# Optimization experiments

Measured on AMD Instinct MI355X. Metric: run time of the kernel, lower is better.

Reference implementation:

```python
import jax, jax.numpy as jnp
import numpy as np

B, T, D = 64, 512, 256   # batch, time, input feat
H = 256                  # LSTM hidden (features)


def setup_inputs() -> dict:
    key = jax.random.key(0)
    ks = jax.random.split(key, 16)
    s = lambda k, shp, fan: jax.random.normal(k, shp, jnp.float32) / np.sqrt(fan)
    return {
        "x":  jax.random.normal(ks[0], (B, T, D), jnp.float32),
        # LSTM params: fused gates order (i, f, g, o)
        "Wi": s(ks[1], (D, 4 * H), D),
        "Wh": s(ks[2], (H, 4 * H), H),
        "b":  jnp.zeros((4 * H,), jnp.float32),
        # single-head attention (head_dim = H)
        "Wq": s(ks[3], (H, H), H), "bq": jnp.zeros((H,), jnp.float32),
        "Wk": s(ks[4], (H, H), H), "bk": jnp.zeros((H,), jnp.float32),
        "Wv": s(ks[5], (H, H), H), "bv": jnp.zeros((H,), jnp.float32),
        "Wo": s(ks[6], (H, H), H), "bo": jnp.zeros((H,), jnp.float32),
        # MLP head
        "W1": s(ks[7], (H, 32), H), "b1": jnp.zeros((32,), jnp.float32),
        "W2": s(ks[8], (32, 3), 32), "b2": jnp.zeros((3,), jnp.float32),
    }


def _lstm_scan(x, Wi, Wh, b):
    # Precompute input-to-hidden projection for all timesteps (batched GEMM)
    xg = jnp.einsum('btd,dg->btg', x, Wi) + b          # [B,T,4H]
    c0 = jnp.zeros((x.shape[0], Wh.shape[0]), x.dtype)
    h0 = jnp.zeros_like(c0)

    def step(carry, xg_t):
        c, h = carry
        g = xg_t + h @ Wh                               # [B,4H]
        i, f, gg, o = jnp.split(g, 4, axis=-1)          # flax gate order i,f,g,o
        c = jax.nn.sigmoid(f) * c + jax.nn.sigmoid(i) * jnp.tanh(gg)
        h = jax.nn.sigmoid(o) * jnp.tanh(c)
        return (c, h), h

    (_, _), hs = jax.lax.scan(step, (c0, h0), jnp.swapaxes(xg, 0, 1))
    return jnp.swapaxes(hs, 0, 1)                       # [B,T,H]


def reference(x, Wi, Wh, b, Wq, bq, Wk, bk, Wv, bv, Wo, bo, W1, b1, W2, b2):
    h = _lstm_scan(x, Wi, Wh, b)                        # [B,T,H]
    # single-head dot-product attention (self-attention)
    q = h @ Wq + bq
    k = h @ Wk + bk
    v = h @ Wv + bv
    scale = 1.0 / np.sqrt(q.shape[-1]).astype(np.float32)
    scores = jnp.einsum('bqd,bkd->bqk', q * scale, k)   # [B,T,T]
    attn = jax.nn.softmax(scores, axis=-1)
    o = jnp.einsum('bqk,bkd->bqd', attn, v)
    o = o @ Wo + bo                                     # output projection
    # head on first timestep
    z = jax.nn.relu(o[:, 0, :] @ W1 + b1)
    return z @ W2 + b2                                  # [B,3]
```

## Files before the change

### kernel.cpp

```cpp
#include <hip/hip_runtime.h>
#include <hip/hip_bf16.h>


typedef __attribute__((ext_vector_type(8))) short short8;
typedef __attribute__((ext_vector_type(4))) float float4v;

__device__ __forceinline__ unsigned short f2bf(float f) {
  unsigned u = __builtin_bit_cast(unsigned, f);
  return (unsigned short)((u + 0x7fffu + ((u >> 16) & 1u)) >> 16);
}
__device__ __forceinline__ float bf2f(unsigned short h) {
  return __builtin_bit_cast(float, ((unsigned)h) << 16);
}
__device__ __forceinline__ float bcl(unsigned u) {
  return __builtin_bit_cast(float, u << 16);
}
__device__ __forceinline__ float bch(unsigned u) {
  return __builtin_bit_cast(float, u & 0xffff0000u);
}
__device__ __forceinline__ float sigm(float x) { return 1.f / (1.f + __expf(-x)); }
__device__ __forceinline__ float tanh_f(float x) { return 1.f - 2.f / (1.f + __expf(2.f * x)); }

__global__ void prep_x(const float* __restrict__ x, unsigned short* __restrict__ xbf) {
  size_t i = ((size_t)blockIdx.x * 256 + threadIdx.x) * 4;
  float4 v = *(const float4*)&x[i];
  unsigned long long pk = (unsigned long long)f2bf(v.x)
                        | ((unsigned long long)f2bf(v.y) << 16)
                        | ((unsigned long long)f2bf(v.z) << 32)
                        | ((unsigned long long)f2bf(v.w) << 48);
  *(unsigned long long*)&xbf[i] = pk;
}

__global__ void prep_wit(const float* __restrict__ Wi, unsigned short* __restrict__ WiT) {
  size_t i = ((size_t)blockIdx.x * 256 + threadIdx.x) * 4;
  float4 v = *(const float4*)&Wi[i];
  int k = (int)(i >> 10), n = (int)(i & 1023);
  WiT[(size_t)(n + 0) * 256 + k] = f2bf(v.x);
  WiT[(size_t)(n + 1) * 256 + k] = f2bf(v.y);
  WiT[(size_t)(n + 2) * 256 + k] = f2bf(v.z);
  WiT[(size_t)(n + 3) * 256 + k] = f2bf(v.w);
}

__global__ void init_hx(unsigned long long* __restrict__ hx) {
  hx[(size_t)blockIdx.x * 256 + threadIdx.x] = 0xffffffff00000000ULL;
}

#define XKP 40
__global__ __launch_bounds__(256) void xg_gemm(const unsigned short* __restrict__ xbf,
                                               const unsigned short* __restrict__ WiT,
                                               const float* __restrict__ bias,
                                               unsigned short* __restrict__ xg) {
  __shared__ unsigned short As[128 * XKP];
  __shared__ unsigned short Bs[128 * XKP];
  const int tid = threadIdx.x;
  const int n0 = blockIdx.x * 128, m0 = blockIdx.y * 128;
  const int wave = tid >> 6, lane = tid & 63, quad = lane >> 4, l16 = lane & 15;
  const int wm = wave >> 1, wn = wave & 1;

  float4v acc[4][4];
#pragma unroll
  for (int i = 0; i < 4; ++i)
#pragma unroll
    for (int j = 0; j < 4; ++j) acc[i][j] = (float4v){0.f, 0.f, 0.f, 0.f};

  const int rr = tid >> 2, c8 = (tid & 3) * 8;
  for (int k0 = 0; k0 < 256; k0 += 32) {
#pragma unroll
    for (int pp = 0; pp < 2; ++pp) {
      int r = pp * 64 + rr;
      *(uint4*)&As[r * XKP + c8] = *(const uint4*)&xbf[(size_t)(m0 + r) * 256 + k0 + c8];
      *(uint4*)&Bs[r * XKP + c8] = *(const uint4*)&WiT[(size_t)(n0 + r) * 256 + k0 + c8];
    }
    __syncthreads();
#pragma unroll
    for (int mt = 0; mt < 4; ++mt) {
      short8 af = *(const short8*)&As[(wm * 64 + mt * 16 + l16) * XKP + quad * 8];
#pragma unroll
      for (int nt = 0; nt < 4; ++nt) {
        short8 bf = *(const short8*)&Bs[(wn * 64 + nt * 16 + l16) * XKP + quad * 8];
        acc[mt][nt] = __builtin_amdgcn_mfma_f32_16x16x32_bf16(af, bf, acc[mt][nt], 0, 0, 0);
      }
    }
    __syncthreads();
  }
#pragma unroll
  for (int nt = 0; nt < 4; ++nt) {
    int col = n0 + wn * 64 + nt * 16 + l16;
    int gate = col >> 8, ggx = (col >> 4) & 15, ul = col & 15;
    float bv = bias[col];
#pragma unroll
    for (int mt = 0; mt < 4; ++mt) {
#pragma unroll
      for (int r = 0; r < 4; ++r) {
        int row = m0 + wm * 64 + mt * 16 + quad * 4 + r;
        int b = row >> 9, t = row & 511;
        xg[(((size_t)ggx * 64 + b) * 512 + t) * 64 + gate * 16 + ul] =
            f2bf(acc[mt][nt][r] + bv);
      }
    }
  }
}

#define KP2 264
__global__ __launch_bounds__(256) void lstm_scan(const float* __restrict__ Wh,
                                                 const unsigned short* __restrict__ xgbuf,
                                                 unsigned short* __restrict__ hout,
                                                 unsigned long long* __restrict__ hx) {
  __shared__ unsigned short WhS[64 * KP2];
  __shared__ unsigned short hA[16 * KP2];
  __shared__ float preS[16 * 68];
  __shared__ float cS[256];
  const int tid = threadIdx.x;
  const int wg = blockIdx.x, bg = wg >> 4, gg = wg & 15;
  const int wave = tid >> 6, lane = tid & 63, quad = lane >> 4, l16 = lane & 15;

  {
    int uu = tid & 15, kh = tid >> 4;
#pragma unroll
    for (int gt = 0; gt < 4; ++gt)
      for (int kb = 0; kb < 16; ++kb) {
        int k = kb * 16 + kh;
        WhS[(gt * 16 + uu) * KP2 + k] = f2bf(Wh[(size_t)k * 1024 + gt * 256 + gg * 16 + uu]);
      }
  }
  for (int i = tid; i < 16 * KP2; i += 256) hA[i] = 0;
  cS[tid] = 0.f;
  __syncthreads();

  const int b_loc = tid >> 4, u_loc = tid & 15;
  const int bgb = bg * 16 + b_loc;
  const int u_glob = gg * 16 + u_loc;
  const int nrow = wave * 16 + l16;
  const unsigned short* xgp0 = xgbuf + ((size_t)(gg * 64 + bgb) * 512) * 64 + u_loc;

  unsigned short xi = xgp0[0], xf = xgp0[16], xG = xgp0[32], xo = xgp0[48];

  for (int t = 0; t < 512; ++t) {
    float4v acc = (float4v){0.f, 0.f, 0.f, 0.f};
#pragma unroll
    for (int kt = 0; kt < 8; ++kt) {
      short8 af = *(const short8*)&hA[l16 * KP2 + kt * 32 + quad * 8];
      short8 bf = *(const short8*)&WhS[nrow * KP2 + kt * 32 + quad * 8];
      acc = __builtin_amdgcn_mfma_f32_16x16x32_bf16(af, bf, acc, 0, 0, 0);
    }
#pragma unroll
    for (int r = 0; r < 4; ++r)
      preS[(quad * 4 + r) * 68 + wave * 16 + l16] = acc[r];

    int tn = (t < 511) ? t + 1 : t;
    const unsigned short* xgn = xgp0 + (size_t)tn * 64;
    unsigned short nxi = xgn[0], nxf = xgn[16], nxG = xgn[32], nxo = xgn[48];
    __syncthreads();

    float gi = preS[b_loc * 68 + 0 * 16 + u_loc] + bf2f(xi);
    float gf = preS[b_loc * 68 + 1 * 16 + u_loc] + bf2f(xf);
    float gG = preS[b_loc * 68 + 2 * 16 + u_loc] + bf2f(xG);
    float go = preS[b_loc * 68 + 3 * 16 + u_loc] + bf2f(xo);
    float c = sigm(gf) * cS[tid] + sigm(gi) * tanh_f(gG);
    cS[tid] = c;
    float h = sigm(go) * tanh_f(c);
    unsigned hb = (unsigned)f2bf(h);
    hA[b_loc * KP2 + u_glob] = (unsigned short)hb;

    const unsigned tg = (unsigned)t;
    unsigned v1 = __shfl_down((int)hb, 1);
    if ((u_loc & 1) == 0) {
      unsigned d0 = hb | (v1 << 16);
      unsigned long long val = (unsigned long long)d0 | ((unsigned long long)tg << 32);
      unsigned long long* dst =
          hx + (((size_t)(t & 1) * 64 + bgb) * 128 + (u_glob >> 1));
      __hip_atomic_store(dst, val, __ATOMIC_RELAXED, __HIP_MEMORY_SCOPE_AGENT);
      *(unsigned*)&hout[((size_t)bgb * 512 + t) * 256 + u_glob] = d0;
    }

    {
      int b2 = tid >> 4, grp = tid & 15;
      if (grp != gg) {
        const unsigned long long* base =
            hx + (((size_t)(t & 1) * 64 + bg * 16 + b2) * 128 + grp * 8);
        unsigned long long w[8];
        int guard = 0;
        bool ok;
        do {
          ok = true;
#pragma unroll
          for (int i = 0; i < 8; ++i) {
            w[i] = __hip_atomic_load(&base[i], __ATOMIC_RELAXED,
                                     __HIP_MEMORY_SCOPE_AGENT);
            ok &= ((unsigned)(w[i] >> 32) == tg);
          }
        } while (!ok && ++guard < (1 << 20));
        int u0 = grp * 16;
#pragma unroll
        for (int i = 0; i < 8; ++i)
          *(unsigned*)&hA[b2 * KP2 + u0 + 2 * i] = (unsigned)w[i];
      }
    }
    xi = nxi; xf = nxf; xG = nxG; xo = nxo;
    __syncthreads();
  }
}

__global__ __launch_bounds__(256) void attn_qu(const unsigned short* __restrict__ hout,
                                               const float* __restrict__ Wq,
                                               const float* __restrict__ bq,
                                               const float* __restrict__ Wk,
                                               const float* __restrict__ bk,
                                               float* __restrict__ us,
                                               float* __restrict__ cbuf) {
  __shared__ float h0S[256], q0S[256], red[256];
  const int b = blockIdx.x, tid = threadIdx.x;
  h0S[tid] = bf2f(hout[(size_t)b * 512 * 256 + tid]);
  __syncthreads();
  float a = 0.f;
  for (int k = 0; k < 256; ++k) a += h0S[k] * Wq[(size_t)k * 256 + tid];
  q0S[tid] = a + bq[tid];
  __syncthreads();
  red[tid] = q0S[tid] * bk[tid];
  __syncthreads();
  for (int s = 128; s > 0; s >>= 1) {
    if (tid < s) red[tid] += red[tid + s];
    __syncthreads();
  }
  if (tid == 0) cbuf[b] = 0.0625f * red[0];
  float acc = 0.f;
  const float* wr = &Wk[(size_t)tid * 256];
  for (int e = 0; e < 256; e += 4) {
    float4 w = *(const float4*)&wr[e];
    acc += w.x * q0S[e] + w.y * q0S[e + 1] + w.z * q0S[e + 2] + w.w * q0S[e + 3];
  }
  us[b * 256 + tid] = 0.0625f * acc;
}

__global__ __launch_bounds__(256) void attn_sm(const unsigned short* __restrict__ hout,
                                               const float* __restrict__ us,
                                               const float* __restrict__ cbuf,
                                               float* __restrict__ hbar) {
  __shared__ float sS[512], red[256], hb4[4][256];
  const int b = blockIdx.x, tid = threadIdx.x, wave = tid >> 6, lane = tid & 63;
  const size_t hb_base = (size_t)b * 512 * 256;
  const float u0 = us[b * 256 + lane * 4 + 0], u1 = us[b * 256 + lane * 4 + 1];
  const float u2 = us[b * 256 + lane * 4 + 2], u3 = us[b * 256 + lane * 4 + 3];
  const float cbv = cbuf[b];
  for (int i = 0; i < 128; ++i) {
    int t = i * 4 + wave;
    unsigned long long hv = *(const unsigned long long*)&hout[hb_base + (size_t)t * 256 + lane * 4];
    unsigned lo = (unsigned)hv, hi = (unsigned)(hv >> 32);
    float p = u0 * bcl(lo) + u1 * bch(lo) + u2 * bcl(hi) + u3 * bch(hi);
    for (int m = 1; m < 64; m <<= 1) p += __shfl_xor(p, m, 64);
    if (lane == 0) sS[t] = p + cbv;
  }
  __syncthreads();
  red[tid] = fmaxf(sS[tid], sS[tid + 256]);
  __syncthreads();
  for (int s = 128; s > 0; s >>= 1) {
    if (tid < s) red[tid] = fmaxf(red[tid], red[tid + s]);
    __syncthreads();
  }
  float mx = red[0];
  __syncthreads();
  float e0 = __expf(sS[tid] - mx), e1 = __expf(sS[tid + 256] - mx);
  sS[tid] = e0; sS[tid + 256] = e1;
  red[tid] = e0 + e1;
  __syncthreads();
  for (int s = 128; s > 0; s >>= 1) {
    if (tid < s) red[tid] += red[tid + s];
    __syncthreads();
  }
  float inv = 1.f / red[0];
  float a0 = 0.f, a1 = 0.f, a2 = 0.f, a3 = 0.f;
  const int d0 = lane * 4;
  for (int i = 0; i < 128; ++i) {
    int t = wave * 128 + i;
    float w = sS[t];
    unsigned long long hv = *(const unsigned long long*)&hout[hb_base + (size_t)t * 256 + d0];
    unsigned lo = (unsigned)hv, hi = (unsigned)(hv >> 32);
    a0 += w * bcl(lo); a1 += w * bch(lo); a2 += w * bcl(hi); a3 += w * bch(hi);
  }
  hb4[wave][d0] = a0; hb4[wave][d0 + 1] = a1; hb4[wave][d0 + 2] = a2; hb4[wave][d0 + 3] = a3;
  __syncthreads();
  hbar[b * 256 + tid] = (hb4[0][tid] + hb4[1][tid] + hb4[2][tid] + hb4[3][tid]) * inv;
}

__global__ __launch_bounds__(256) void head_k(const float* __restrict__ hbar,
                                              const float* __restrict__ Wv, const float* __restrict__ bv,
                                              const float* __restrict__ Wo, const float* __restrict__ bo,
                                              const float* __restrict__ W1, const float* __restrict__ b1,
                                              const float* __restrict__ W2, const float* __restrict__ b2,
                                              float* __restrict__ out) {
  __shared__ float hS[256], oS[256], o1S[256], zS[32];
  const int b = blockIdx.x, tid = threadIdx.x;
  hS[tid] = hbar[b * 256 + tid];
  __syncthreads();
  float a = 0.f;
  for (int k = 0; k < 256; ++k) a += hS[k] * Wv[(size_t)k * 256 + tid];
  oS[tid] = a + bv[tid];
  __syncthreads();
  a = 0.f;
  for (int k = 0; k < 256; ++k) a += oS[k] * Wo[(size_t)k * 256 + tid];
  o1S[tid] = a + bo[tid];
  __syncthreads();
  if (tid < 32) {
    a = 0.f;
    for (int k = 0; k < 256; ++k) a += o1S[k] * W1[k * 32 + tid];
    zS[tid] = fmaxf(a + b1[tid], 0.f);
  }
  __syncthreads();
  if (tid < 3) {
    a = 0.f;
    for (int j = 0; j < 32; ++j) a += zS[j] * W2[j * 3 + tid];
    out[b * 3 + tid] = a + b2[tid];
  }
}

extern "C" void kernel_launch(void* const* d_in, const int* in_sizes, int n_in,
                              void* d_out, int out_size, void* d_ws, size_t ws_size,
                              hipStream_t stream) {
  const float* x  = (const float*)d_in[0];
  const float* Wi = (const float*)d_in[1];
  const float* Wh = (const float*)d_in[2];
  const float* bG = (const float*)d_in[3];
  const float* Wq = (const float*)d_in[4];
  const float* bq = (const float*)d_in[5];
  const float* Wk = (const float*)d_in[6];
  const float* bk = (const float*)d_in[7];
  const float* Wv = (const float*)d_in[8];
  const float* bv = (const float*)d_in[9];
  const float* Wo = (const float*)d_in[10];
  const float* bo = (const float*)d_in[11];
  const float* W1 = (const float*)d_in[12];
  const float* b1 = (const float*)d_in[13];
  const float* W2 = (const float*)d_in[14];
  const float* b2 = (const float*)d_in[15];
  float* out = (float*)d_out;
  char* ws = (char*)d_ws;

  unsigned short* xg    = (unsigned short*)(ws);
  unsigned short* hout  = (unsigned short*)(ws + 67108864);
  unsigned short* xbf   = (unsigned short*)(ws + 83886080);
  unsigned short* WiT   = (unsigned short*)(ws + 100663296);
  unsigned long long* hx = (unsigned long long*)(ws + 101187584);
  float*          us    = (float*)(ws + 101318656);
  float*          cbuf  = (float*)(ws + 101384192);
  float*          hbar  = (float*)(ws + 101385216);

  prep_x<<<dim3(8192), dim3(256), 0, stream>>>(x, xbf);
  prep_wit<<<dim3(256), dim3(256), 0, stream>>>(Wi, WiT);
  init_hx<<<dim3(64), dim3(256), 0, stream>>>(hx);
  xg_gemm<<<dim3(8, 256), dim3(256), 0, stream>>>(xbf, WiT, bG, xg);
  lstm_scan<<<dim3(64), dim3(256), 0, stream>>>(Wh, xg, hout, hx);
  attn_qu<<<dim3(64), dim3(256), 0, stream>>>(hout, Wq, bq, Wk, bk, us, cbuf);
  attn_sm<<<dim3(64), dim3(256), 0, stream>>>(hout, us, cbuf, hbar);
  head_k<<<dim3(64), dim3(256), 0, stream>>>(hbar, Wv, bv, Wo, bo, W1, b1, W2, b2, out);
}
```

Measured before the change: 1.409 ms.

## Repartition LSTM scan to 16 blocks with register-resident Wh and in-register gates

The recurrent scan now runs on 16 workgroups instead of 64. Each block owns 64 hidden units across all four gates for a 16-batch group and keeps its Wh slice as MFMA B-fragments in registers rather than LDS. The xg layout is changed to interleave the four gates per unit, so each lane computes the cell update directly from its accumulators and keeps c in registers. This removes the preS/cS LDS round trip and one barrier, and cuts the number of peers each block must poll through global memory per step. In exchange each block does four times the MFMA work per step, uses far fewer CUs, and carries high register pressure from the 32 resident fragments.

```diff
diff --git a/kernel.cpp b/kernel.cpp
--- a/kernel.cpp
+++ b/kernel.cpp
@@ -86,117 +86,131 @@
 #pragma unroll
   for (int nt = 0; nt < 4; ++nt) {
     int col = n0 + wn * 64 + nt * 16 + l16;
-    int gate = col >> 8, ggx = (col >> 4) & 15, ul = col & 15;
+    int gate = col >> 8, gu = col & 255;
     float bv = bias[col];
 #pragma unroll
     for (int mt = 0; mt < 4; ++mt) {
 #pragma unroll
       for (int r = 0; r < 4; ++r) {
-        int row = m0 + wm * 64 + mt * 16 + quad * 4 + r;
-        int b = row >> 9, t = row & 511;
-        xg[(((size_t)ggx * 64 + b) * 512 + t) * 64 + gate * 16 + ul] =
-            f2bf(acc[mt][nt][r] + bv);
+        int m = m0 + wm * 64 + mt * 16 + quad * 4 + r;
+        xg[(size_t)m * 1024 + gu * 4 + gate] = f2bf(acc[mt][nt][r] + bv);
       }
     }
   }
 }
 
 #define KP2 264
-__global__ __launch_bounds__(256) void lstm_scan(const float* __restrict__ Wh,
-                                                 const unsigned short* __restrict__ xgbuf,
-                                                 unsigned short* __restrict__ hout,
-                                                 unsigned long long* __restrict__ hx) {
-  __shared__ unsigned short WhS[64 * KP2];
+__global__ __launch_bounds__(256, 1) void lstm_scan(const float* __restrict__ Wh,
+                                                    const unsigned short* __restrict__ xgbuf,
+                                                    unsigned short* __restrict__ hout,
+                                                    unsigned long long* __restrict__ hx) {
+  __shared__ unsigned short stage[64 * KP2];
   __shared__ unsigned short hA[16 * KP2];
-  __shared__ float preS[16 * 68];
-  __shared__ float cS[256];
   const int tid = threadIdx.x;
-  const int wg = blockIdx.x, bg = wg >> 4, gg = wg & 15;
+  const int blk = blockIdx.x, bg = blk >> 2, ug = blk & 3;
   const int wave = tid >> 6, lane = tid & 63, quad = lane >> 4, l16 = lane & 15;
-
-  {
-    int uu = tid & 15, kh = tid >> 4;
-#pragma unroll
-    for (int gt = 0; gt < 4; ++gt)
-      for (int kb = 0; kb < 16; ++kb) {
-        int k = kb * 16 + kh;
-        WhS[(gt * 16 + uu) * KP2 + k] = f2bf(Wh[(size_t)k * 1024 + gt * 256 + gg * 16 + uu]);
-      }
+  const int gu = ug * 64 + wave * 16 + l16;
+
+  short8 Bfrag[4][8];
+#pragma unroll
+  for (int g = 0; g < 4; ++g) {
+    for (int idx = tid; idx < 64 * 256; idx += 256) {
+      int u = idx & 63, k = idx >> 6;
+      stage[u * KP2 + k] = f2bf(Wh[(size_t)k * 1024 + g * 256 + ug * 64 + u]);
+    }
+    __syncthreads();
+#pragma unroll
+    for (int kt = 0; kt < 8; ++kt)
+      Bfrag[g][kt] = *(const short8*)&stage[(wave * 16 + l16) * KP2 + kt * 32 + quad * 8];
+    __syncthreads();
   }
   for (int i = tid; i < 16 * KP2; i += 256) hA[i] = 0;
-  cS[tid] = 0.f;
-  __syncthreads();
-
-  const int b_loc = tid >> 4, u_loc = tid & 15;
-  const int bgb = bg * 16 + b_loc;
-  const int u_glob = gg * 16 + u_loc;
-  const int nrow = wave * 16 + l16;
-  const unsigned short* xgp0 = xgbuf + ((size_t)(gg * 64 + bgb) * 512) * 64 + u_loc;
-
-  unsigned short xi = xgp0[0], xf = xgp0[16], xG = xgp0[32], xo = xgp0[48];
+  __syncthreads();
+
+  float creg[4] = {0.f, 0.f, 0.f, 0.f};
+
+  const unsigned short* xgb[4];
+#pragma unroll
+  for (int r = 0; r < 4; ++r)
+    xgb[r] = xgbuf + ((size_t)(bg * 16 + quad * 4 + r) * 512) * 1024 + gu * 4;
+
+  const int b2 = tid >> 4, pidx = tid & 15;
+  const int batchg = bg * 16 + b2;
+  int gw[6];
+#pragma unroll
+  for (int j = 0; j < 6; ++j) {
+    int f = pidx * 6 + j;
+    gw[j] = f + ((f >= ug * 32) ? 32 : 0);
+  }
+
+  ushort4 xv[4];
+#pragma unroll
+  for (int r = 0; r < 4; ++r) xv[r] = *(const ushort4*)xgb[r];
 
   for (int t = 0; t < 512; ++t) {
-    float4v acc = (float4v){0.f, 0.f, 0.f, 0.f};
+    float4v acc[4];
+#pragma unroll
+    for (int g = 0; g < 4; ++g) acc[g] = (float4v){0.f, 0.f, 0.f, 0.f};
 #pragma unroll
     for (int kt = 0; kt < 8; ++kt) {
       short8 af = *(const short8*)&hA[l16 * KP2 + kt * 32 + quad * 8];
-      short8 bf = *(const short8*)&WhS[nrow * KP2 + kt * 32 + quad * 8];
-      acc = __builtin_amdgcn_mfma_f32_16x16x32_bf16(af, bf, acc, 0, 0, 0);
-    }
-#pragma unroll
-    for (int r = 0; r < 4; ++r)
-      preS[(quad * 4 + r) * 68 + wave * 16 + l16] = acc[r];
+#pragma unroll
+      for (int g = 0; g < 4; ++g)
+        acc[g] = __builtin_amdgcn_mfma_f32_16x16x32_bf16(af, Bfrag[g][kt], acc[g], 0, 0, 0);
+    }
 
     int tn = (t < 511) ? t + 1 : t;
-    const unsigned short* xgn = xgp0 + (size_t)tn * 64;
-    unsigned short nxi = xgn[0], nxf = xgn[16], nxG = xgn[32], nxo = xgn[48];
-    __syncthreads();
-
-    float gi = preS[b_loc * 68 + 0 * 16 + u_loc] + bf2f(xi);
-    float gf = preS[b_loc * 68 + 1 * 16 + u_loc] + bf2f(xf);
-    float gG = preS[b_loc * 68 + 2 * 16 + u_loc] + bf2f(xG);
-    float go = preS[b_loc * 68 + 3 * 16 + u_loc] + bf2f(xo);
-    float c = sigm(gf) * cS[tid] + sigm(gi) * tanh_f(gG);
-    cS[tid] = c;
-    float h = sigm(go) * tanh_f(c);
-    unsigned hb = (unsigned)f2bf(h);
-    hA[b_loc * KP2 + u_glob] = (unsigned short)hb;
+    ushort4 nxv[4];
+#pragma unroll
+    for (int r = 0; r < 4; ++r) nxv[r] = *(const ushort4*)(xgb[r] + (size_t)tn * 1024);
+
+    unsigned hb[4];
+#pragma unroll
+    for (int r = 0; r < 4; ++r) {
+      float gi = acc[0][r] + bf2f(xv[r].x);
+      float gf = acc[1][r] + bf2f(xv[r].y);
+      float gG = acc[2][r] + bf2f(xv[r].z);
+      float go = acc[3][r] + bf2f(xv[r].w);
+      float c = sigm(gf) * creg[r] + sigm(gi) * tanh_f(gG);
+      creg[r] = c;
+      hb[r] = (unsigned)f2bf(sigm(go) * tanh_f(c));
+    }
+    __syncthreads();
 
     const unsigned tg = (unsigned)t;
-    unsigned v1 = __shfl_down((int)hb, 1);
-    if ((u_loc & 1) == 0) {
-      unsigned d0 = hb | (v1 << 16);
-      unsigned long long val = (unsigned long long)d0 | ((unsigned long long)tg << 32);
-      unsigned long long* dst =
-          hx + (((size_t)(t & 1) * 64 + bgb) * 128 + (u_glob >> 1));
-      __hip_atomic_store(dst, val, __ATOMIC_RELAXED, __HIP_MEMORY_SCOPE_AGENT);
-      *(unsigned*)&hout[((size_t)bgb * 512 + t) * 256 + u_glob] = d0;
+#pragma unroll
+    for (int r = 0; r < 4; ++r) {
+      int b = bg * 16 + quad * 4 + r;
+      hA[(quad * 4 + r) * KP2 + gu] = (unsigned short)hb[r];
+      hout[((size_t)b * 512 + t) * 256 + gu] = (unsigned short)hb[r];
+      unsigned nb = (unsigned)__shfl_down((int)hb[r], 1);
+      if ((l16 & 1) == 0) {
+        unsigned long long val =
+            (unsigned long long)(hb[r] | (nb << 16)) | ((unsigned long long)tg << 32);
+        __hip_atomic_store(&hx[((size_t)(t & 1) * 64 + b) * 128 + (gu >> 1)], val,
+                           __ATOMIC_RELAXED, __HIP_MEMORY_SCOPE_AGENT);
+      }
     }
 
     {
-      int b2 = tid >> 4, grp = tid & 15;
-      if (grp != gg) {
-        const unsigned long long* base =
-            hx + (((size_t)(t & 1) * 64 + bg * 16 + b2) * 128 + grp * 8);
-        unsigned long long w[8];
-        int guard = 0;
-        bool ok;
-        do {
-          ok = true;
-#pragma unroll
-          for (int i = 0; i < 8; ++i) {
-            w[i] = __hip_atomic_load(&base[i], __ATOMIC_RELAXED,
-                                     __HIP_MEMORY_SCOPE_AGENT);
-            ok &= ((unsigned)(w[i] >> 32) == tg);
-          }
-        } while (!ok && ++guard < (1 << 20));
-        int u0 = grp * 16;
-#pragma unroll
-        for (int i = 0; i < 8; ++i)
-          *(unsigned*)&hA[b2 * KP2 + u0 + 2 * i] = (unsigned)w[i];
-      }
-    }
-    xi = nxi; xf = nxf; xG = nxG; xo = nxo;
+      const unsigned long long* base = hx + ((size_t)(t & 1) * 64 + batchg) * 128;
+      unsigned long long w[6];
+      int guard = 0;
+      bool ok;
+      do {
+        ok = true;
+#pragma unroll
+        for (int j = 0; j < 6; ++j) {
+          w[j] = __hip_atomic_load(&base[gw[j]], __ATOMIC_RELAXED,
+                                   __HIP_MEMORY_SCOPE_AGENT);
+          ok &= ((unsigned)(w[j] >> 32) == tg);
+        }
+      } while (!ok && ++guard < (1 << 20));
+#pragma unroll
+      for (int j = 0; j < 6; ++j)
+        *(unsigned*)&hA[b2 * KP2 + gw[j] * 2] = (unsigned)w[j];
+    }
+    xv[0] = nxv[0]; xv[1] = nxv[1]; xv[2] = nxv[2]; xv[3] = nxv[3];
     __syncthreads();
   }
 }
@@ -348,7 +362,7 @@
   prep_wit<<<dim3(256), dim3(256), 0, stream>>>(Wi, WiT);
   init_hx<<<dim3(64), dim3(256), 0, stream>>>(hx);
   xg_gemm<<<dim3(8, 256), dim3(256), 0, stream>>>(xbf, WiT, bG, xg);
-  lstm_scan<<<dim3(64), dim3(256), 0, stream>>>(Wh, xg, hout, hx);
+  lstm_scan<<<dim3(16), dim3(256), 0, stream>>>(Wh, xg, hout, hx);
   attn_qu<<<dim3(64), dim3(256), 0, stream>>>(hout, Wq, bq, Wk, bk, us, cbuf);
   attn_sm<<<dim3(64), dim3(256), 0, stream>>>(hout, us, cbuf, hbar);
   head_k<<<dim3(64), dim3(256), 0, stream>>>(hbar, Wv, bv, Wo, bo, W1, b1, W2, b2, out);
```

Result: slower. 1.563 ms (+10.9%).
